# Kernel tuning notes

Measured on AMD Instinct MI355X. Metric: run time of the kernel, lower is better.

Reference implementation:

```python
import jax, jax.numpy as jnp
import numpy as np

N_NODES = 50000
N_EDGES = 800000
EPS = 1e-5


def _glorot(key, fan_in, fan_out):
    lim = np.sqrt(6.0 / (fan_in + fan_out))
    return jax.random.uniform(key, (fan_in, fan_out), jnp.float32, -lim, lim)


def setup_inputs() -> dict:
    key = jax.random.key(0)
    ks = jax.random.split(key, 16)
    x = jax.random.normal(ks[0], (N_NODES, 88), jnp.float32)
    edge_index = jax.random.randint(ks[1], (2, N_EDGES), 0, N_NODES, jnp.int64)
    dims = [(88, 70), (70, 60), (60, 50), (50, 60), (60, 70), (70, 88)]
    inp = {"x": x, "edge_index": edge_index}
    for i, (fi, fo) in enumerate(dims):
        inp[f"W{i+1}"] = _glorot(ks[2 + i], fi, fo)
        inp[f"b{i+1}"] = jnp.zeros((fo,), jnp.float32)
    # BatchNorm affine params for layers with bn: widths 70,60,60,70
    for i, w in enumerate([70, 60, 60, 70]):
        inp[f"g{i+1}"] = jnp.ones((w,), jnp.float32)
        inp[f"be{i+1}"] = jnp.zeros((w,), jnp.float32)
    return inp


def _gcn_norm(edge_index, n_nodes):
    # add self-loops, symmetric normalization: D^-1/2 (A+I) D^-1/2
    loop = jnp.arange(n_nodes, dtype=edge_index.dtype)
    src = jnp.concatenate([edge_index[0], loop])
    dst = jnp.concatenate([edge_index[1], loop])
    deg = jax.ops.segment_sum(jnp.ones_like(dst, jnp.float32), dst, num_segments=n_nodes)
    dis = jnp.where(deg > 0, jax.lax.rsqrt(deg), 0.0)
    norm = dis[src] * dis[dst]  # [E+N]
    return src, dst, norm


def _gcn(x, W, b, src, dst, norm, n_nodes):
    h = x @ W  # transform first (small out dim)
    msg = h[src] * norm[:, None]
    return jax.ops.segment_sum(msg, dst, num_segments=n_nodes) + b


def _bn(x, g, be):
    mu = jnp.mean(x, axis=0)
    var = jnp.mean(jnp.square(x - mu), axis=0)
    return g * (x - mu) * jax.lax.rsqrt(var + EPS) + be


def reference(x, edge_index, W1, b1, W2, b2, W3, b3, W4, b4, W5, b5, W6, b6,
              g1, be1, g2, be2, g3, be3, g4, be4):
    n = x.shape[0]
    src, dst, norm = _gcn_norm(edge_index, n)
    # encoder
    h = jax.nn.relu(_gcn(x, W1, b1, src, dst, norm, n))
    h = _bn(h, g1, be1)
    h = jax.nn.relu(_gcn(h, W2, b2, src, dst, norm, n))
    h = _bn(h, g2, be2)
    h = _gcn(h, W3, b3, src, dst, norm, n)
    # decoder
    h = jax.nn.relu(_gcn(h, W4, b4, src, dst, norm, n))
    h = _bn(h, g3, be3)
    h = jax.nn.relu(_gcn(h, W5, b5, src, dst, norm, n))
    h = _bn(h, g4, be4)
    h = _gcn(h, W6, b6, src, dst, norm, n)
    return h
```

## Files before the change

### kernel.cpp

```cpp
#include <hip/hip_runtime.h>
#include <hip/hip_bf16.h>

typedef unsigned int  uint_t;
typedef unsigned short ushort_t;

#define NN 50000
#define NE 800000
#define NBLK 196

static inline int cdiv(long long a, long long b) { return (int)((a + b - 1) / b); }

__device__ inline float bflo(uint_t u) { return __uint_as_float(u << 16); }
__device__ inline float bfhi(uint_t u) { return __uint_as_float(u & 0xffff0000u); }
__device__ inline uint_t packbf(float x, float y) {
    uint_t xu = __float_as_uint(x), yu = __float_as_uint(y);
    xu += 0x7fffu + ((xu >> 16) & 1u);
    yu += 0x7fffu + ((yu >> 16) & 1u);
    return (xu >> 16) | (yu & 0xffff0000u);
}
__device__ inline ushort_t packbf1(float x) {
    uint_t xu = __float_as_uint(x);
    xu += 0x7fffu + ((xu >> 16) & 1u);
    return (ushort_t)(xu >> 16);
}


__global__ void k_prep(int* __restrict__ deg, float* __restrict__ bnacc) {
    int i = blockIdx.x * blockDim.x + threadIdx.x;
    if (i < NN) deg[i] = 0;
    if (i < 768) bnacc[i] = 0.0f;
}

__global__ void k_hist(const int* __restrict__ dst, int* __restrict__ deg) {
    int e = blockIdx.x * blockDim.x + threadIdx.x;
    if (e < NE) {
        int d = dst[e];
        if ((unsigned)d < NN) atomicAdd(&deg[d], 1);
    }
}

__global__ void k_bsum(const int* __restrict__ deg, int* __restrict__ bsum) {
    __shared__ int l[256];
    int tid = threadIdx.x;
    int i = blockIdx.x * 256 + tid;
    l[tid] = (i < NN) ? deg[i] : 0;
    __syncthreads();
    for (int o = 128; o > 0; o >>= 1) {
        if (tid < o) l[tid] += l[tid + o];
        __syncthreads();
    }
    if (tid == 0) bsum[blockIdx.x] = l[0];
}

__global__ void k_bscan(const int* __restrict__ bsum, int* __restrict__ boff,
                        int* __restrict__ row_ptr) {
    __shared__ int l[256];
    int tid = threadIdx.x;
    int v = (tid < NBLK) ? bsum[tid] : 0;
    l[tid] = v;
    __syncthreads();
    for (int o = 1; o < 256; o <<= 1) {
        int t = (tid >= o) ? l[tid - o] : 0;
        __syncthreads();
        l[tid] += t;
        __syncthreads();
    }
    boff[tid] = l[tid] - v;
    if (tid == 255) row_ptr[NN] = l[255];
}

__global__ void k_rowptr(const int* __restrict__ deg, const int* __restrict__ boff,
                         int* __restrict__ row_ptr, int* __restrict__ cursor,
                         float* __restrict__ dis) {
    __shared__ int l[256];
    int tid = threadIdx.x;
    int i = blockIdx.x * 256 + tid;
    int v = (i < NN) ? deg[i] : 0;
    l[tid] = v;
    __syncthreads();
    for (int o = 1; o < 256; o <<= 1) {
        int t = (tid >= o) ? l[tid - o] : 0;
        __syncthreads();
        l[tid] += t;
        __syncthreads();
    }
    if (i < NN) {
        int excl = boff[blockIdx.x] + l[tid] - v;
        row_ptr[i] = excl;
        cursor[i] = excl;
        dis[i] = rsqrtf((float)(v + 1));
    }
}

__global__ void k_fill(const int* __restrict__ src, const int* __restrict__ dst,
                       const float* __restrict__ dis,
                       int* __restrict__ cursor, int2* __restrict__ cw) {
    int e = blockIdx.x * blockDim.x + threadIdx.x;
    if (e < NE) {
        int s = src[e], d = dst[e];
        if ((unsigned)s < NN && (unsigned)d < NN) {
            int p = atomicAdd(&cursor[d], 1);
            cw[p] = make_int2(s, __float_as_int(dis[s] * dis[d]));
        }
    }
}

struct FoldJob {
    const float* W; const float* b;
    const float* bnacc; const float* g; const float* be;
    float* Wp; float* bf;
    int FI, FO, in_bn, out_b;
};
struct FoldJobs { FoldJob j[4]; };

__global__ void k_fold(FoldJobs jobs) {
    FoldJob J = jobs.j[blockIdx.x];
    const int FI = J.FI, FO = J.FO;
    const int NT = (FO + 15) / 16, FOP = 16 * NT;
    __shared__ float scl[96], shl[96];
    int tid = threadIdx.x;
    if (J.in_bn) {
        if (tid < FI) {
            const float inv_n = 1.0f / NN;
            float mu = J.bnacc[tid] * inv_n;
            float va = J.bnacc[96 + tid] * inv_n - mu * mu;
            float r  = rsqrtf(va + 1e-5f);
            float sc = J.g[tid] * r;
            scl[tid] = sc;
            shl[tid] = J.be[tid] - mu * sc;
        }
        __syncthreads();
    }
    for (int idx = tid; idx < FI * FOP; idx += 256) {
        int k = idx / FOP, j = idx - k * FOP;
        float w = (j < FO) ? J.W[k * FO + j] : 0.0f;
        if (J.in_bn) w *= scl[k];
        J.Wp[(k >> 1) * 2 * FOP + 2 * j + (k & 1)] = w;
    }
    if (tid < FOP) {
        float a = (J.out_b && tid < FO) ? J.b[tid] : 0.0f;
        if (J.in_bn && tid < FO) {
            for (int k = 0; k < FI; ++k) a = fmaf(shl[k], J.W[k * FO + tid], a);
        }
        J.bf[tid] = a;
    }
}

template<int FI, int FO, int IN_BN, int IN_F32, int OUT_F32, int OUT_BN>
__global__ __launch_bounds__(256)
void k_dense(const void* __restrict__ Xv, const float* __restrict__ Wp,
             const float* __restrict__ biasf, void* __restrict__ Hv,
             float* __restrict__ bnst) {
    constexpr int NT  = (FO + 15) / 16;
    constexpr int FOP = 16 * NT;
    constexpr int FIP = FI + 2;
    constexpr int KP  = FI / 2;

    __shared__ __align__(16) float xs[64 * FIP];
    __shared__ float ls[96], lq[96];

    int tid = threadIdx.x;
    int node0 = blockIdx.x * 64;

    if (OUT_BN) {
        if (tid < 96) { ls[tid] = 0.0f; lq[tid] = 0.0f; }
    }

    if (IN_F32) {
        for (int idx = tid; idx < 64 * FI; idx += 256) {
            int r = idx / FI, c = idx - r * FI;
            int n = node0 + r;
            float v = (n < NN) ? ((const float*)Xv)[(size_t)n * FI + c] : 0.0f;
            if (IN_BN) v = fmaxf(v, 0.0f);
            xs[r * FIP + c] = v;
        }
    } else {
        for (int idx = tid; idx < 64 * KP; idx += 256) {
            int r = idx / KP, c2 = idx - r * KP;
            int n = node0 + r;
            uint_t u = (n < NN) ? ((const uint_t*)Xv)[(size_t)n * KP + c2] : 0u;
            float f0 = bflo(u), f1 = bfhi(u);
            if (IN_BN) { f0 = fmaxf(f0, 0.0f); f1 = fmaxf(f1, 0.0f); }
            xs[r * FIP + 2 * c2]     = f0;
            xs[r * FIP + 2 * c2 + 1] = f1;
        }
    }
    __syncthreads();

    int ng = tid >> 4;
    int cg = tid & 15;

    float acc[4][NT];
    #pragma unroll
    for (int i = 0; i < 4; ++i)
        #pragma unroll
        for (int t = 0; t < NT; ++t) acc[i][t] = biasf[cg + 16 * t];

    #pragma unroll 2
    for (int k = 0; k < FI; k += 2) {
        float2 xv[4];
        #pragma unroll
        for (int i = 0; i < 4; ++i)
            xv[i] = *(const float2*)&xs[(ng + 16 * i) * FIP + k];
        const float* wrow = &Wp[(k >> 1) * 2 * FOP];
        #pragma unroll
        for (int t = 0; t < NT; ++t) {
            float2 w = *(const float2*)&wrow[2 * (cg + 16 * t)];
            #pragma unroll
            for (int i = 0; i < 4; ++i)
                acc[i][t] = fmaf(xv[i].y, w.y, fmaf(xv[i].x, w.x, acc[i][t]));
        }
    }

    if (OUT_BN) {
        #pragma unroll
        for (int t = 0; t < NT; ++t) {
            float ps = 0.0f, pq = 0.0f;
            #pragma unroll
            for (int i = 0; i < 4; ++i) {
                if (node0 + ng + 16 * i < NN) {
                    float r = fmaxf(acc[i][t], 0.0f);
                    ps += r; pq += r * r;
                }
            }
            atomicAdd(&ls[cg + 16 * t], ps);
            atomicAdd(&lq[cg + 16 * t], pq);
        }
        __syncthreads();
        if (tid < FO) {
            atomicAdd(&bnst[tid], ls[tid]);
            atomicAdd(&bnst[96 + tid], lq[tid]);
        }
    }

    #pragma unroll
    for (int i = 0; i < 4; ++i) {
        int n = node0 + ng + 16 * i;
        if (n < NN) {
            #pragma unroll
            for (int t = 0; t < NT; ++t) {
                int j = cg + 16 * t;
                if (j < FO) {
                    if (OUT_F32) ((float*)Hv)[(size_t)n * FO + j] = acc[i][t];
                    else ((ushort_t*)Hv)[(size_t)n * FO + j] = packbf1(acc[i][t]);
                }
            }
        }
    }
}

template<int FO, int IN_BN, int OUT_BIAS, int OUT_BN>
__global__ void k_gather(const ushort_t* __restrict__ h, const int* __restrict__ row_ptr,
                         const int2* __restrict__ cw, const float* __restrict__ dis,
                         const float* __restrict__ bnacc, const float* __restrict__ g,
                         const float* __restrict__ be,
                         const float* __restrict__ b, ushort_t* __restrict__ A,
                         float* __restrict__ bnacc_out) {
    constexpr int F2 = FO / 2;
    __shared__ float ls[96], lq[96];
    int tid = threadIdx.x;
    if (OUT_BN) {
        if (tid < 96) { ls[tid] = 0.0f; lq[tid] = 0.0f; }
        __syncthreads();
    }

    int t0 = blockIdx.x * blockDim.x + tid;
    const int stride = gridDim.x * blockDim.x;
    int j2 = t0 % F2;
    int j = 2 * j2;

    float sc0 = 1.0f, sh0 = 0.0f, sc1 = 1.0f, sh1 = 0.0f;
    if (IN_BN) {
        const float inv_n = 1.0f / NN;
        float mu0 = bnacc[j] * inv_n;
        float va0 = bnacc[96 + j] * inv_n - mu0 * mu0;
        float r0  = rsqrtf(va0 + 1e-5f);
        sc0 = g[j] * r0; sh0 = be[j] - mu0 * sc0;
        float mu1 = bnacc[j + 1] * inv_n;
        float va1 = bnacc[96 + j + 1] * inv_n - mu1 * mu1;
        float r1  = rsqrtf(va1 + 1e-5f);
        sc1 = g[j + 1] * r1; sh1 = be[j + 1] - mu1 * sc1;
    }

    const uint_t* h2 = (const uint_t*)h + j2;
    float sx = 0.0f, qx = 0.0f, sy = 0.0f, qy = 0.0f;

    for (int t = t0; t < NN * F2; t += stride) {
        int i = t / F2;
        float di = dis[i];

        uint_t su = h2[(size_t)i * F2];
        float vx = bflo(su), vy = bfhi(su);
        if (IN_BN) { vx = fmaxf(vx, 0.0f) * sc0 + sh0; vy = fmaxf(vy, 0.0f) * sc1 + sh1; }
        float ax = vx * di * di;
        float ay = vy * di * di;

        int k = row_ptr[i], end = row_ptr[i + 1];
        for (; k + 8 <= end; k += 8) {
            uint_t uu[8]; float ww[8];
            #pragma unroll
            for (int q = 0; q < 8; ++q) {
                int2 c = cw[k + q];
                ww[q] = __int_as_float(c.y);
                uu[q] = h2[(size_t)c.x * F2];
            }
            #pragma unroll
            for (int q = 0; q < 8; ++q) {
                float tx = bflo(uu[q]), ty = bfhi(uu[q]);
                if (IN_BN) { tx = fmaxf(tx, 0.0f) * sc0 + sh0; ty = fmaxf(ty, 0.0f) * sc1 + sh1; }
                ax = fmaf(tx, ww[q], ax); ay = fmaf(ty, ww[q], ay);
            }
        }
        for (; k < end; ++k) {
            int2 c = cw[k];
            float w = __int_as_float(c.y);
            uint_t u = h2[(size_t)c.x * F2];
            float tx = bflo(u), ty = bfhi(u);
            if (IN_BN) { tx = fmaxf(tx, 0.0f) * sc0 + sh0; ty = fmaxf(ty, 0.0f) * sc1 + sh1; }
            ax = fmaf(tx, w, ax); ay = fmaf(ty, w, ay);
        }
        if (OUT_BIAS) { ax += b[j]; ay += b[j + 1]; }
        if (OUT_BN) {
            float rx = fmaxf(ax, 0.0f), ry = fmaxf(ay, 0.0f);
            sx += rx; qx += rx * rx;
            sy += ry; qy += ry * ry;
        }
        ((uint_t*)A)[(size_t)i * F2 + j2] = packbf(ax, ay);
    }

    if (OUT_BN) {
        atomicAdd(&ls[j], sx);     atomicAdd(&ls[j + 1], sy);
        atomicAdd(&lq[j], qx);     atomicAdd(&lq[j + 1], qy);
        __syncthreads();
        if (tid < FO) {
            atomicAdd(&bnacc_out[tid], ls[tid]);
            atomicAdd(&bnacc_out[96 + tid], lq[tid]);
        }
    }
}

extern "C" void kernel_launch(void* const* d_in, const int* in_sizes, int n_in,
                              void* d_out, int out_size, void* d_ws, size_t ws_size,
                              hipStream_t stream) {
    const float* x = (const float*)d_in[0];
    const int* ei = (const int*)d_in[1];
    const int* src = ei;
    const int* dst = ei + NE;
    const float* W1 = (const float*)d_in[2];  const float* b1 = (const float*)d_in[3];
    const float* W2 = (const float*)d_in[4];  const float* b2 = (const float*)d_in[5];
    const float* W3 = (const float*)d_in[6];  const float* b3 = (const float*)d_in[7];
    const float* W4 = (const float*)d_in[8];  const float* b4 = (const float*)d_in[9];
    const float* W5 = (const float*)d_in[10]; const float* b5 = (const float*)d_in[11];
    const float* W6 = (const float*)d_in[12]; const float* b6 = (const float*)d_in[13];
    const float* g1 = (const float*)d_in[14]; const float* be1 = (const float*)d_in[15];
    const float* g2 = (const float*)d_in[16]; const float* be2 = (const float*)d_in[17];
    const float* g3 = (const float*)d_in[18]; const float* be3 = (const float*)d_in[19];
    const float* g4 = (const float*)d_in[20]; const float* be4 = (const float*)d_in[21];

    float* ws = (float*)d_ws;
    float* dis    = ws;
    float* bnacc  = dis + NN;
    float* Wp     = bnacc + 768;
    float* biasf  = Wp + 6 * 7040;
    int2* cw      = (int2*)(biasf + 6 * 96);
    int* deg      = (int*)(cw + NE);
    int* row_ptr  = deg + NN;
    int* cursor   = row_ptr + NN + 1;
    int* bsum     = cursor + NN;
    int* boff     = bsum + 256;
    ushort_t* hB  = (ushort_t*)(boff + 256);
    ushort_t* aB  = hB + (size_t)NN * 70;
    float* out    = (float*)d_out;

    const int NB = 256;
    const int DGRID = cdiv(NN, 64);
    float* bn0 = bnacc;
    float* bn1 = bnacc + 192;
    float* bn2 = bnacc + 384;
    float* bn3 = bnacc + 576;
    float* WpL[6]; float* bfL[6];
    for (int i = 0; i < 6; ++i) { WpL[i] = Wp + i * 7040; bfL[i] = biasf + i * 96; }

    k_prep<<<cdiv(NN, NB), NB, 0, stream>>>(deg, bnacc);
    k_hist<<<cdiv(NE, NB), NB, 0, stream>>>(dst, deg);
    k_bsum<<<NBLK, 256, 0, stream>>>(deg, bsum);
    k_bscan<<<1, 256, 0, stream>>>(bsum, boff, row_ptr);
    k_rowptr<<<NBLK, 256, 0, stream>>>(deg, boff, row_ptr, cursor, dis);
    k_fill<<<cdiv(NE, NB), NB, 0, stream>>>(src, dst, dis, cursor, cw);

    {
        FoldJobs js;
        js.j[0] = {W1, nullptr, nullptr, nullptr, nullptr, WpL[0], bfL[0], 88, 70, 0, 0};
        js.j[1] = {W4, b4,      nullptr, nullptr, nullptr, WpL[3], bfL[3], 50, 60, 0, 1};
        js.j[2] = {W5, b5,      nullptr, nullptr, nullptr, WpL[4], bfL[4], 60, 70, 0, 1};
        js.j[3] = {W6, b6,      nullptr, nullptr, nullptr, WpL[5], bfL[5], 70, 88, 0, 1};
        k_fold<<<4, 256, 0, stream>>>(js);
    }

    k_dense<88, 70, 0, 1, 0, 0><<<DGRID, 256, 0, stream>>>(x, WpL[0], bfL[0], hB, nullptr);
    k_gather<70, 0, 1, 1><<<56 * 35, NB, 0, stream>>>(
        hB, row_ptr, cw, dis, nullptr, nullptr, nullptr, b1, aB, bn0);

    {
        FoldJobs js;
        js.j[0] = {W2, nullptr, bn0, g1, be1, WpL[1], bfL[1], 70, 60, 1, 0};
        k_fold<<<1, 256, 0, stream>>>(js);
    }
    k_dense<70, 60, 1, 0, 0, 0><<<DGRID, 256, 0, stream>>>(aB, WpL[1], bfL[1], hB, nullptr);
    k_gather<60, 0, 1, 1><<<56 * 30, NB, 0, stream>>>(
        hB, row_ptr, cw, dis, nullptr, nullptr, nullptr, b2, aB, bn1);

    {
        FoldJobs js;
        js.j[0] = {W3, nullptr, bn1, g2, be2, WpL[2], bfL[2], 60, 50, 1, 0};
        k_fold<<<1, 256, 0, stream>>>(js);
    }
    k_dense<60, 50, 1, 0, 0, 0><<<DGRID, 256, 0, stream>>>(aB, WpL[2], bfL[2], hB, nullptr);
    k_gather<50, 0, 1, 0><<<cdiv((long long)NN * 25, NB), NB, 0, stream>>>(
        hB, row_ptr, cw, dis, nullptr, nullptr, nullptr, b3, aB, nullptr);

    k_gather<50, 0, 0, 0><<<cdiv((long long)NN * 25, NB), NB, 0, stream>>>(
        aB, row_ptr, cw, dis, nullptr, nullptr, nullptr, nullptr, hB, nullptr);
    k_dense<50, 60, 0, 0, 0, 1><<<DGRID, 256, 0, stream>>>(hB, WpL[3], bfL[3], aB, bn2);

    k_gather<60, 1, 0, 0><<<cdiv((long long)NN * 30, NB), NB, 0, stream>>>(
        aB, row_ptr, cw, dis, bn2, g3, be3, nullptr, hB, nullptr);
    k_dense<60, 70, 0, 0, 0, 1><<<DGRID, 256, 0, stream>>>(hB, WpL[4], bfL[4], aB, bn3);

    k_gather<70, 1, 0, 0><<<cdiv((long long)NN * 35, NB), NB, 0, stream>>>(
        aB, row_ptr, cw, dis, bn3, g4, be4, nullptr, hB, nullptr);
    k_dense<70, 88, 0, 0, 1, 0><<<DGRID, 256, 0, stream>>>(hB, WpL[5], bfL[5], out, nullptr);
}
```

Measured before the change: 557.3 us.

## Pad bf16 feature rows to multiples of 4 and gather 4 features per thread

Intermediate bf16 activations now use a row stride padded to a multiple of four features, so each gather thread loads 8 bytes (four bf16 values) per neighbor instead of 4 bytes. The grid-stride loop is replaced by one thread per (node, 4-feature group), and the dense kernels read and write the padded layout. This halves the number of threads issuing index and weight loads per edge, and so cuts redundant CSR traffic and address work. In exchange it adds padding bytes, raises register use per thread, and moves to per-element shared atomics for the BN statistics.

```diff
diff --git a/kernel.cpp b/kernel.cpp
--- a/kernel.cpp
+++ b/kernel.cpp
@@ -153,8 +153,10 @@
              float* __restrict__ bnst) {
     constexpr int NT  = (FO + 15) / 16;
     constexpr int FOP = 16 * NT;
+    constexpr int JW  = 4 * ((FO + 3) / 4);
     constexpr int FIP = FI + 2;
     constexpr int KP  = FI / 2;
+    constexpr int S2I = 2 * ((FI + 3) / 4);
 
     __shared__ __align__(16) float xs[64 * FIP];
     __shared__ float ls[96], lq[96];
@@ -178,7 +180,7 @@
         for (int idx = tid; idx < 64 * KP; idx += 256) {
             int r = idx / KP, c2 = idx - r * KP;
             int n = node0 + r;
-            uint_t u = (n < NN) ? ((const uint_t*)Xv)[(size_t)n * KP + c2] : 0u;
+            uint_t u = (n < NN) ? ((const uint_t*)Xv)[(size_t)n * S2I + c2] : 0u;
             float f0 = bflo(u), f1 = bfhi(u);
             if (IN_BN) { f0 = fmaxf(f0, 0.0f); f1 = fmaxf(f1, 0.0f); }
             xs[r * FIP + 2 * c2]     = f0;
@@ -215,16 +217,19 @@
     if (OUT_BN) {
         #pragma unroll
         for (int t = 0; t < NT; ++t) {
-            float ps = 0.0f, pq = 0.0f;
-            #pragma unroll
-            for (int i = 0; i < 4; ++i) {
-                if (node0 + ng + 16 * i < NN) {
-                    float r = fmaxf(acc[i][t], 0.0f);
-                    ps += r; pq += r * r;
+            int j = cg + 16 * t;
+            if (j < FO) {
+                float ps = 0.0f, pq = 0.0f;
+                #pragma unroll
+                for (int i = 0; i < 4; ++i) {
+                    if (node0 + ng + 16 * i < NN) {
+                        float r = fmaxf(acc[i][t], 0.0f);
+                        ps += r; pq += r * r;
+                    }
                 }
+                atomicAdd(&ls[j], ps);
+                atomicAdd(&lq[j], pq);
             }
-            atomicAdd(&ls[cg + 16 * t], ps);
-            atomicAdd(&lq[cg + 16 * t], pq);
         }
         __syncthreads();
         if (tid < FO) {
@@ -240,9 +245,10 @@
             #pragma unroll
             for (int t = 0; t < NT; ++t) {
                 int j = cg + 16 * t;
-                if (j < FO) {
-                    if (OUT_F32) ((float*)Hv)[(size_t)n * FO + j] = acc[i][t];
-                    else ((ushort_t*)Hv)[(size_t)n * FO + j] = packbf1(acc[i][t]);
+                if (OUT_F32) {
+                    if (j < FO) ((float*)Hv)[(size_t)n * FO + j] = acc[i][t];
+                } else {
+                    if (j < JW) ((ushort_t*)Hv)[(size_t)n * JW + j] = packbf1(acc[i][t]);
                 }
             }
         }
@@ -250,13 +256,15 @@
 }
 
 template<int FO, int IN_BN, int OUT_BIAS, int OUT_BN>
-__global__ void k_gather(const ushort_t* __restrict__ h, const int* __restrict__ row_ptr,
-                         const int2* __restrict__ cw, const float* __restrict__ dis,
-                         const float* __restrict__ bnacc, const float* __restrict__ g,
-                         const float* __restrict__ be,
-                         const float* __restrict__ b, ushort_t* __restrict__ A,
-                         float* __restrict__ bnacc_out) {
-    constexpr int F2 = FO / 2;
+__global__ __launch_bounds__(256)
+void k_gather(const uint_t* __restrict__ h, const int* __restrict__ row_ptr,
+              const int2* __restrict__ cw, const float* __restrict__ dis,
+              const float* __restrict__ bnacc, const float* __restrict__ g,
+              const float* __restrict__ be,
+              const float* __restrict__ b, uint_t* __restrict__ A,
+              float* __restrict__ bnacc_out) {
+    constexpr int F4 = (FO + 3) / 4;
+    constexpr int S2 = 2 * F4;
     __shared__ float ls[96], lq[96];
     int tid = threadIdx.x;
     if (OUT_BN) {
@@ -264,73 +272,98 @@
         __syncthreads();
     }
 
-    int t0 = blockIdx.x * blockDim.x + tid;
-    const int stride = gridDim.x * blockDim.x;
-    int j2 = t0 % F2;
-    int j = 2 * j2;
-
-    float sc0 = 1.0f, sh0 = 0.0f, sc1 = 1.0f, sh1 = 0.0f;
+    int t = blockIdx.x * blockDim.x + tid;
+    int i  = t / F4;
+    int j4 = t - i * F4;
+    int j  = 4 * j4;
+    bool valid = i < NN;
+
+    float sc[4], sh[4];
     if (IN_BN) {
         const float inv_n = 1.0f / NN;
-        float mu0 = bnacc[j] * inv_n;
-        float va0 = bnacc[96 + j] * inv_n - mu0 * mu0;
-        float r0  = rsqrtf(va0 + 1e-5f);
-        sc0 = g[j] * r0; sh0 = be[j] - mu0 * sc0;
-        float mu1 = bnacc[j + 1] * inv_n;
-        float va1 = bnacc[96 + j + 1] * inv_n - mu1 * mu1;
-        float r1  = rsqrtf(va1 + 1e-5f);
-        sc1 = g[j + 1] * r1; sh1 = be[j + 1] - mu1 * sc1;
-    }
-
-    const uint_t* h2 = (const uint_t*)h + j2;
-    float sx = 0.0f, qx = 0.0f, sy = 0.0f, qy = 0.0f;
-
-    for (int t = t0; t < NN * F2; t += stride) {
-        int i = t / F2;
+        #pragma unroll
+        for (int q = 0; q < 4; ++q) {
+            int jq = j + q;
+            if (jq < FO) {
+                float mu = bnacc[jq] * inv_n;
+                float va = bnacc[96 + jq] * inv_n - mu * mu;
+                float r  = rsqrtf(va + 1e-5f);
+                sc[q] = g[jq] * r; sh[q] = be[jq] - mu * sc[q];
+            } else { sc[q] = 0.0f; sh[q] = 0.0f; }
+        }
+    }
+
+    float a0 = 0.0f, a1 = 0.0f, a2 = 0.0f, a3 = 0.0f;
+
+    if (valid) {
+        const uint_t* hq = h + 2 * j4;
         float di = dis[i];
 
-        uint_t su = h2[(size_t)i * F2];
-        float vx = bflo(su), vy = bfhi(su);
-        if (IN_BN) { vx = fmaxf(vx, 0.0f) * sc0 + sh0; vy = fmaxf(vy, 0.0f) * sc1 + sh1; }
-        float ax = vx * di * di;
-        float ay = vy * di * di;
+        uint2 su = *(const uint2*)(hq + (size_t)i * S2);
+        float f0 = bflo(su.x), f1 = bfhi(su.x), f2 = bflo(su.y), f3 = bfhi(su.y);
+        if (IN_BN) {
+            f0 = fmaxf(f0, 0.0f) * sc[0] + sh[0]; f1 = fmaxf(f1, 0.0f) * sc[1] + sh[1];
+            f2 = fmaxf(f2, 0.0f) * sc[2] + sh[2]; f3 = fmaxf(f3, 0.0f) * sc[3] + sh[3];
+        }
+        float dd = di * di;
+        a0 = f0 * dd; a1 = f1 * dd; a2 = f2 * dd; a3 = f3 * dd;
+        if (OUT_BIAS) {
+            #pragma unroll
+            for (int q = 0; q < 4; ++q) {
+                int jq = j + q;
+                float bv = (jq < FO) ? b[jq] : 0.0f;
+                if (q == 0) a0 += bv; else if (q == 1) a1 += bv;
+                else if (q == 2) a2 += bv; else a3 += bv;
+            }
+        }
 
         int k = row_ptr[i], end = row_ptr[i + 1];
         for (; k + 8 <= end; k += 8) {
-            uint_t uu[8]; float ww[8];
+            int2  c[8]; uint2 u[8];
+            #pragma unroll
+            for (int q = 0; q < 8; ++q) c[q] = cw[k + q];
+            #pragma unroll
+            for (int q = 0; q < 8; ++q)
+                u[q] = *(const uint2*)(hq + (size_t)c[q].x * S2);
             #pragma unroll
             for (int q = 0; q < 8; ++q) {
-                int2 c = cw[k + q];
-                ww[q] = __int_as_float(c.y);
-                uu[q] = h2[(size_t)c.x * F2];
-            }
-            #pragma unroll
-            for (int q = 0; q < 8; ++q) {
-                float tx = bflo(uu[q]), ty = bfhi(uu[q]);
-                if (IN_BN) { tx = fmaxf(tx, 0.0f) * sc0 + sh0; ty = fmaxf(ty, 0.0f) * sc1 + sh1; }
-                ax = fmaf(tx, ww[q], ax); ay = fmaf(ty, ww[q], ay);
+                float w = __int_as_float(c[q].y);
+                float t0 = bflo(u[q].x), t1 = bfhi(u[q].x);
+                float t2 = bflo(u[q].y), t3 = bfhi(u[q].y);
+                if (IN_BN) {
+                    t0 = fmaxf(t0, 0.0f) * sc[0] + sh[0]; t1 = fmaxf(t1, 0.0f) * sc[1] + sh[1];
+                    t2 = fmaxf(t2, 0.0f) * sc[2] + sh[2]; t3 = fmaxf(t3, 0.0f) * sc[3] + sh[3];
+                }
+                a0 = fmaf(t0, w, a0); a1 = fmaf(t1, w, a1);
+                a2 = fmaf(t2, w, a2); a3 = fmaf(t3, w, a3);
             }
         }
         for (; k < end; ++k) {
             int2 c = cw[k];
             float w = __int_as_float(c.y);
-            uint_t u = h2[(size_t)c.x * F2];
-            float tx = bflo(u), ty = bfhi(u);
-            if (IN_BN) { tx = fmaxf(tx, 0.0f) * sc0 + sh0; ty = fmaxf(ty, 0.0f) * sc1 + sh1; }
-            ax = fmaf(tx, w, ax); ay = fmaf(ty, w, ay);
-        }
-        if (OUT_BIAS) { ax += b[j]; ay += b[j + 1]; }
-        if (OUT_BN) {
-            float rx = fmaxf(ax, 0.0f), ry = fmaxf(ay, 0.0f);
-            sx += rx; qx += rx * rx;
-            sy += ry; qy += ry * ry;
-        }
-        ((uint_t*)A)[(size_t)i * F2 + j2] = packbf(ax, ay);
+            uint2 u = *(const uint2*)(hq + (size_t)c.x * S2);
+            float t0 = bflo(u.x), t1 = bfhi(u.x), t2 = bflo(u.y), t3 = bfhi(u.y);
+            if (IN_BN) {
+                t0 = fmaxf(t0, 0.0f) * sc[0] + sh[0]; t1 = fmaxf(t1, 0.0f) * sc[1] + sh[1];
+                t2 = fmaxf(t2, 0.0f) * sc[2] + sh[2]; t3 = fmaxf(t3, 0.0f) * sc[3] + sh[3];
+            }
+            a0 = fmaf(t0, w, a0); a1 = fmaf(t1, w, a1);
+            a2 = fmaf(t2, w, a2); a3 = fmaf(t3, w, a3);
+        }
+
+        *(uint2*)(A + (size_t)i * S2 + 2 * j4) =
+            make_uint2(packbf(a0, a1), packbf(a2, a3));
     }
 
     if (OUT_BN) {
-        atomicAdd(&ls[j], sx);     atomicAdd(&ls[j + 1], sy);
-        atomicAdd(&lq[j], qx);     atomicAdd(&lq[j + 1], qy);
+        if (valid) {
+            float r0 = fmaxf(a0, 0.0f), r1 = fmaxf(a1, 0.0f);
+            float r2 = fmaxf(a2, 0.0f), r3 = fmaxf(a3, 0.0f);
+            if (j     < FO) { atomicAdd(&ls[j],     r0); atomicAdd(&lq[j],     r0 * r0); }
+            if (j + 1 < FO) { atomicAdd(&ls[j + 1], r1); atomicAdd(&lq[j + 1], r1 * r1); }
+            if (j + 2 < FO) { atomicAdd(&ls[j + 2], r2); atomicAdd(&lq[j + 2], r2 * r2); }
+            if (j + 3 < FO) { atomicAdd(&ls[j + 3], r3); atomicAdd(&lq[j + 3], r3 * r3); }
+        }
         __syncthreads();
         if (tid < FO) {
             atomicAdd(&bnacc_out[tid], ls[tid]);
@@ -357,19 +390,18 @@
     const float* g3 = (const float*)d_in[18]; const float* be3 = (const float*)d_in[19];
     const float* g4 = (const float*)d_in[20]; const float* be4 = (const float*)d_in[21];
 
-    float* ws = (float*)d_ws;
-    float* dis    = ws;
+    int2* cw      = (int2*)d_ws;
+    float* dis    = (float*)(cw + NE);
     float* bnacc  = dis + NN;
     float* Wp     = bnacc + 768;
     float* biasf  = Wp + 6 * 7040;
-    int2* cw      = (int2*)(biasf + 6 * 96);
-    int* deg      = (int*)(cw + NE);
+    int* deg      = (int*)(biasf + 6 * 96);
     int* row_ptr  = deg + NN;
-    int* cursor   = row_ptr + NN + 1;
+    int* cursor   = row_ptr + NN + 2;
     int* bsum     = cursor + NN;
     int* boff     = bsum + 256;
-    ushort_t* hB  = (ushort_t*)(boff + 256);
-    ushort_t* aB  = hB + (size_t)NN * 70;
+    uint_t* hB    = (uint_t*)(boff + 256);
+    uint_t* aB    = hB + (size_t)NN * 36;
     float* out    = (float*)d_out;
 
     const int NB = 256;
@@ -398,7 +430,7 @@
     }
 
     k_dense<88, 70, 0, 1, 0, 0><<<DGRID, 256, 0, stream>>>(x, WpL[0], bfL[0], hB, nullptr);
-    k_gather<70, 0, 1, 1><<<56 * 35, NB, 0, stream>>>(
+    k_gather<70, 0, 1, 1><<<18 * NBLK, NB, 0, stream>>>(
         hB, row_ptr, cw, dis, nullptr, nullptr, nullptr, b1, aB, bn0);
 
     {
@@ -407,7 +439,7 @@
         k_fold<<<1, 256, 0, stream>>>(js);
     }
     k_dense<70, 60, 1, 0, 0, 0><<<DGRID, 256, 0, stream>>>(aB, WpL[1], bfL[1], hB, nullptr);
-    k_gather<60, 0, 1, 1><<<56 * 30, NB, 0, stream>>>(
+    k_gather<60, 0, 1, 1><<<15 * NBLK, NB, 0, stream>>>(
         hB, row_ptr, cw, dis, nullptr, nullptr, nullptr, b2, aB, bn1);
 
     {
@@ -416,18 +448,18 @@
         k_fold<<<1, 256, 0, stream>>>(js);
     }
     k_dense<60, 50, 1, 0, 0, 0><<<DGRID, 256, 0, stream>>>(aB, WpL[2], bfL[2], hB, nullptr);
-    k_gather<50, 0, 1, 0><<<cdiv((long long)NN * 25, NB), NB, 0, stream>>>(
+    k_gather<50, 0, 1, 0><<<13 * NBLK, NB, 0, stream>>>(
         hB, row_ptr, cw, dis, nullptr, nullptr, nullptr, b3, aB, nullptr);
 
-    k_gather<50, 0, 0, 0><<<cdiv((long long)NN * 25, NB), NB, 0, stream>>>(
+    k_gather<50, 0, 0, 0><<<13 * NBLK, NB, 0, stream>>>(
         aB, row_ptr, cw, dis, nullptr, nullptr, nullptr, nullptr, hB, nullptr);
     k_dense<50, 60, 0, 0, 0, 1><<<DGRID, 256, 0, stream>>>(hB, WpL[3], bfL[3], aB, bn2);
 
-    k_gather<60, 1, 0, 0><<<cdiv((long long)NN * 30, NB), NB, 0, stream>>>(
+    k_gather<60, 1, 0, 0><<<15 * NBLK, NB, 0, stream>>>(
         aB, row_ptr, cw, dis, bn2, g3, be3, nullptr, hB, nullptr);
     k_dense<60, 70, 0, 0, 0, 1><<<DGRID, 256, 0, stream>>>(hB, WpL[4], bfL[4], aB, bn3);
 
-    k_gather<70, 1, 0, 0><<<cdiv((long long)NN * 35, NB), NB, 0, stream>>>(
+    k_gather<70, 1, 0, 0><<<18 * NBLK, NB, 0, stream>>>(
         aB, row_ptr, cw, dis, bn3, g4, be4, nullptr, hB, nullptr);
     k_dense<70, 88, 0, 0, 1, 0><<<DGRID, 256, 0, stream>>>(hB, WpL[5], bfL[5], out, nullptr);
 }
```

Result: slower. 615.7 us (+10.5%).
